# Kernel optimization log

Hardware: AMD Instinct MI355X
Metric: run time of the kernel (lower is better)

The kernel has to match this reference:

```python
import jax, jax.numpy as jnp
import numpy as np

N, D = 8192, 1024
TEMPERATURE = 0.1
EPS = 1e-8

def setup_inputs() -> dict:
    key = jax.random.key(0)
    k1, k2 = jax.random.split(key)
    emb = jax.random.normal(k1, (N, D), dtype=jnp.float32)
    # docstring: embeddings are normalized
    emb = emb / jnp.linalg.norm(emb, axis=1, keepdims=True)
    labels = jax.random.randint(k2, (N,), 0, 2, dtype=jnp.int32)
    return {"embeddings": emb, "labels": labels}

def reference(embeddings, labels):
    lab = labels.astype(embeddings.dtype)            # (N,)
    sim = jnp.matmul(embeddings, embeddings.T) / TEMPERATURE  # (N, N)
    exp_sim = jnp.exp(sim)                           # original uses raw exp (no max-subtract)
    diag = jnp.diagonal(exp_sim)                     # self-similarity exp(1/T)
    # all_sim excludes self; pos_sim = other reference rows (labels==1, j != i)
    all_sum = exp_sim.sum(axis=1) - diag             # (N,)
    pos_sum = exp_sim @ lab - diag * lab             # subtract self only when i is ref
    loss_per_row = -jnp.log(pos_sum / (all_sum + EPS))
    n_ref = lab.sum()
    loss = jnp.sum(jnp.where(lab > 0, loss_per_row, 0.0)) / jnp.maximum(n_ref, 1.0)
    # original returns 0.0 when fewer than 2 reference rows
    return jnp.where(n_ref < 2, jnp.array(0.0, embeddings.dtype), loss)
```

## Files before the change

kernel.cpp:

```cpp
#include <hip/hip_runtime.h>
#include <hip/hip_bf16.h>
#include <cstdint>
#include <cstddef>

#define NROWS 8192
#define DIM   1024
#define BM 128
#define BN 128
#define BK 64
#define INV_T 10.0f
#define EPS 1e-8f

typedef short  bf16x8  __attribute__((ext_vector_type(8)));
typedef float  floatx4 __attribute__((ext_vector_type(4)));

typedef __attribute__((address_space(1))) const void CGV;
typedef __attribute__((address_space(3))) void LV;

__device__ __forceinline__ void async_load16(const void* g, void* l) {
    __builtin_amdgcn_global_load_lds((CGV*)g, (LV*)l, 16, 0, 0);
}

__device__ __forceinline__ unsigned short f2bf_rne(float f) {
    union { float f; unsigned u; } c; c.f = f;
    unsigned u = c.u;
    unsigned r = (u + 0x7fffu + ((u >> 16) & 1u)) >> 16;
    return (unsigned short)r;
}

__global__ __launch_bounds__(256) void convert_kernel(
    const float* __restrict__ in, unsigned short* __restrict__ out)
{
    int i = (blockIdx.x * 256 + threadIdx.x) * 4;
    float4 v = *(const float4*)(in + i);
    ushort4 o;
    o.x = f2bf_rne(v.x);
    o.y = f2bf_rne(v.y);
    o.z = f2bf_rne(v.z);
    o.w = f2bf_rne(v.w);
    *(ushort4*)(out + i) = o;
}

__global__ __launch_bounds__(256, 4) void gemm_fused_kernel(
    const unsigned short* __restrict__ E,
    const int*            __restrict__ labels,
    float*                __restrict__ all_sum,
    float*                __restrict__ pos_sum)
{
    __shared__ __align__(16) unsigned short sA[BM * BK];
    __shared__ __align__(16) unsigned short sB[BN * BK];

    const int tid  = threadIdx.x;
    const int lane = tid & 63;
    const int w    = tid >> 6;
    const int wm   = w >> 1;
    const int wn   = w & 1;
    const int colw = lane & 15;
    const int quad = lane >> 4;

    const int t = blockIdx.x;
    int bi = (int)((sqrtf(8.0f * (float)t + 1.0f) - 1.0f) * 0.5f);
    while ((bi + 1) * (bi + 2) / 2 <= t) ++bi;
    while (bi * (bi + 1) / 2 > t) --bi;
    const int bj = t - bi * (bi + 1) / 2;

    const int rBase = bi * BM;
    const int cBase = bj * BN;
    const bool diag = (bi == bj);

    const int srow  = tid >> 3;
    const int scol  = (((tid & 7) ^ (srow & 7)) << 3);
    const int e0    = tid * 8;

    floatx4 acc[4][4];
    #pragma unroll
    for (int i = 0; i < 4; ++i)
        #pragma unroll
        for (int j = 0; j < 4; ++j)
            acc[i][j] = (floatx4)0.0f;

    const int swz   = colw & 7;
    const int aRow0 = (wm * 64 + colw) * BK;
    const int bRow0 = (wn * 64 + colw) * BK;

    const size_t gA0 = (size_t)(rBase + srow) * DIM + scol;
    const size_t gB0 = (size_t)(cBase + srow) * DIM + scol;
    const size_t rstep = (size_t)32 * DIM;

    for (int k0 = 0; k0 < DIM; k0 += BK) {
        __syncthreads();
        async_load16(E + gA0 + k0,             &sA[e0]);
        async_load16(E + gA0 + rstep + k0,     &sA[e0 + 2048]);
        async_load16(E + gA0 + 2 * rstep + k0, &sA[e0 + 4096]);
        async_load16(E + gA0 + 3 * rstep + k0, &sA[e0 + 6144]);
        async_load16(E + gB0 + k0,             &sB[e0]);
        async_load16(E + gB0 + rstep + k0,     &sB[e0 + 2048]);
        async_load16(E + gB0 + 2 * rstep + k0, &sB[e0 + 4096]);
        async_load16(E + gB0 + 3 * rstep + k0, &sB[e0 + 6144]);
        __syncthreads();

        #pragma unroll
        for (int h = 0; h < 2; ++h) {
            const int cOff = (((h << 2) | quad) ^ swz) << 3;
            bf16x8 aF[4], bF[4];
            #pragma unroll
            for (int mt = 0; mt < 4; ++mt)
                aF[mt] = *(const bf16x8*)&sA[aRow0 + mt * 16 * BK + cOff];
            #pragma unroll
            for (int nt = 0; nt < 4; ++nt)
                bF[nt] = *(const bf16x8*)&sB[bRow0 + nt * 16 * BK + cOff];

            #pragma unroll
            for (int mt = 0; mt < 4; ++mt)
                #pragma unroll
                for (int nt = 0; nt < 4; ++nt)
                    acc[mt][nt] = __builtin_amdgcn_mfma_f32_16x16x32_bf16(
                        aF[mt], bF[nt], acc[mt][nt], 0, 0, 0);
        }
    }

    float labc[4];
    int   gcol[4];
    #pragma unroll
    for (int nt = 0; nt < 4; ++nt) {
        gcol[nt] = cBase + wn * 64 + nt * 16 + colw;
        labc[nt] = (float)labels[gcol[nt]];
    }

    float colAll[4] = {0.f, 0.f, 0.f, 0.f};
    float colPos[4] = {0.f, 0.f, 0.f, 0.f};

    #pragma unroll
    for (int mt = 0; mt < 4; ++mt) {
        const int growBase = rBase + wm * 64 + mt * 16 + quad * 4;
        #pragma unroll
        for (int r = 0; r < 4; ++r) {
            const int grow = growBase + r;
            const float labr = (float)labels[grow];
            float sAll = 0.f, sPos = 0.f;
            #pragma unroll
            for (int nt = 0; nt < 4; ++nt) {
                float ev = __expf(acc[mt][nt][r] * INV_T);
                if (diag && grow == gcol[nt]) ev = 0.0f;
                sAll += ev;
                sPos += ev * labc[nt];
                colAll[nt] += ev;
                colPos[nt] += ev * labr;
            }
            #pragma unroll
            for (int off = 1; off < 16; off <<= 1) {
                sAll += __shfl_xor(sAll, off);
                sPos += __shfl_xor(sPos, off);
            }
            if (colw == 0) {
                atomicAdd(&all_sum[grow], sAll);
                atomicAdd(&pos_sum[grow], sPos);
            }
        }
    }

    if (!diag) {
        #pragma unroll
        for (int nt = 0; nt < 4; ++nt) {
            float a = colAll[nt], p = colPos[nt];
            a += __shfl_xor(a, 16);  p += __shfl_xor(p, 16);
            a += __shfl_xor(a, 32);  p += __shfl_xor(p, 32);
            if (quad == 0) {
                atomicAdd(&all_sum[gcol[nt]], a);
                atomicAdd(&pos_sum[gcol[nt]], p);
            }
        }
    }
}

__global__ __launch_bounds__(1024) void finalize_kernel(
    const float* __restrict__ all_sum,
    const float* __restrict__ pos_sum,
    const int*   __restrict__ labels,
    float*       __restrict__ out)
{
    __shared__ float sSum[1024];
    __shared__ float sCnt[1024];
    const int tid = threadIdx.x;
    float lsum = 0.f, lcnt = 0.f;
    for (int i = tid; i < NROWS; i += 1024) {
        if (labels[i] > 0) {
            float p = pos_sum[i];
            float a = all_sum[i] + EPS;
            lsum += -logf(p / a);
            lcnt += 1.0f;
        }
    }
    sSum[tid] = lsum;
    sCnt[tid] = lcnt;
    __syncthreads();
    for (int s = 512; s > 0; s >>= 1) {
        if (tid < s) { sSum[tid] += sSum[tid + s]; sCnt[tid] += sCnt[tid + s]; }
        __syncthreads();
    }
    if (tid == 0) {
        float n = sCnt[0];
        out[0] = (n < 2.0f) ? 0.0f : sSum[0] / fmaxf(n, 1.0f);
    }
}

extern "C" void kernel_launch(void* const* d_in, const int* in_sizes, int n_in,
                              void* d_out, int out_size, void* d_ws, size_t ws_size,
                              hipStream_t stream) {
    const float* emb    = (const float*)d_in[0];
    const int*   labels = (const int*)d_in[1];
    float*       out    = (float*)d_out;

    unsigned short* Ebf = (unsigned short*)d_ws;
    const size_t embBytes = (size_t)NROWS * DIM * sizeof(unsigned short);
    float* all_sum = (float*)((char*)d_ws + embBytes);
    float* pos_sum = all_sum + NROWS;

    hipMemsetAsync(all_sum, 0, 2 * NROWS * sizeof(float), stream);

    convert_kernel<<<(NROWS * DIM) / (4 * 256), 256, 0, stream>>>(emb, Ebf);

    const int nBlocksTri = (NROWS / BM) * (NROWS / BM + 1) / 2;
    gemm_fused_kernel<<<nBlocksTri, 256, 0, stream>>>(Ebf, labels, all_sum, pos_sum);

    finalize_kernel<<<1, 1024, 0, stream>>>(all_sum, pos_sum, labels, out);
}
```

Measured before the change: 217.5 us.

## Double-buffer LDS tiles with smaller K step and fold accumulator zeroing into convert

The GEMM main loop now keeps two LDS buffers with a K step of 32 instead of 64. It issues the async global-to-LDS loads for the next tile before computing on the current one, using one barrier per iteration instead of two, and the load/read swizzle is reworked to fit the narrower tile. The separate memset of the row-sum accumulators is removed; the convert kernel zeroes them instead, saving one stream operation. In exchange there are twice as many K iterations and barriers, and correctness depends on the barrier waiting for the outstanding async LDS loads.

Result: slower. 235.7 us (+8.4%).

```diff
diff --git a/kernel.cpp b/kernel.cpp
--- a/kernel.cpp
+++ b/kernel.cpp
@@ -7,7 +7,7 @@
 #define DIM   1024
 #define BM 128
 #define BN 128
-#define BK 64
+#define BK 32
 #define INV_T 10.0f
 #define EPS 1e-8f
 
@@ -29,7 +29,8 @@
 }
 
 __global__ __launch_bounds__(256) void convert_kernel(
-    const float* __restrict__ in, unsigned short* __restrict__ out)
+    const float* __restrict__ in, unsigned short* __restrict__ out,
+    float* __restrict__ accum )
 {
     int i = (blockIdx.x * 256 + threadIdx.x) * 4;
     float4 v = *(const float4*)(in + i);
@@ -39,6 +40,8 @@
     o.z = f2bf_rne(v.z);
     o.w = f2bf_rne(v.w);
     *(ushort4*)(out + i) = o;
+    if (blockIdx.x < (2 * NROWS) / 256)
+        accum[blockIdx.x * 256 + threadIdx.x] = 0.0f;
 }
 
 __global__ __launch_bounds__(256, 4) void gemm_fused_kernel(
@@ -47,8 +50,8 @@
     float*                __restrict__ all_sum,
     float*                __restrict__ pos_sum)
 {
-    __shared__ __align__(16) unsigned short sA[BM * BK];
-    __shared__ __align__(16) unsigned short sB[BN * BK];
+    __shared__ __align__(16) unsigned short sA[2][BM * BK];
+    __shared__ __align__(16) unsigned short sB[2][BN * BK];
 
     const int tid  = threadIdx.x;
     const int lane = tid & 63;
@@ -68,9 +71,9 @@
     const int cBase = bj * BN;
     const bool diag = (bi == bj);
 
-    const int srow  = tid >> 3;
-    const int scol  = (((tid & 7) ^ (srow & 7)) << 3);
-    const int e0    = tid * 8;
+    const int srow = tid >> 2;
+    const int scol = (((tid & 3) ^ ((tid >> 3) & 3)) << 3);
+    const int e0   = tid * 8;
 
     floatx4 acc[4][4];
     #pragma unroll
@@ -79,44 +82,46 @@
         for (int j = 0; j < 4; ++j)
             acc[i][j] = (floatx4)0.0f;
 
-    const int swz   = colw & 7;
+    const int swz   = (colw >> 1) & 3;
+    const int cOff  = ((quad ^ swz) << 3);
     const int aRow0 = (wm * 64 + colw) * BK;
     const int bRow0 = (wn * 64 + colw) * BK;
 
     const size_t gA0 = (size_t)(rBase + srow) * DIM + scol;
     const size_t gB0 = (size_t)(cBase + srow) * DIM + scol;
-    const size_t rstep = (size_t)32 * DIM;
-
-    for (int k0 = 0; k0 < DIM; k0 += BK) {
+    const size_t rstep = (size_t)64 * DIM;
+
+    async_load16(E + gA0,         &sA[0][e0]);
+    async_load16(E + gA0 + rstep, &sA[0][e0 + 2048]);
+    async_load16(E + gB0,         &sB[0][e0]);
+    async_load16(E + gB0 + rstep, &sB[0][e0 + 2048]);
+
+    #pragma unroll 2
+    for (int it = 0; it < DIM / BK; ++it) {
+        const int cur = it & 1;
         __syncthreads();
-        async_load16(E + gA0 + k0,             &sA[e0]);
-        async_load16(E + gA0 + rstep + k0,     &sA[e0 + 2048]);
-        async_load16(E + gA0 + 2 * rstep + k0, &sA[e0 + 4096]);
-        async_load16(E + gA0 + 3 * rstep + k0, &sA[e0 + 6144]);
-        async_load16(E + gB0 + k0,             &sB[e0]);
-        async_load16(E + gB0 + rstep + k0,     &sB[e0 + 2048]);
-        async_load16(E + gB0 + 2 * rstep + k0, &sB[e0 + 4096]);
-        async_load16(E + gB0 + 3 * rstep + k0, &sB[e0 + 6144]);
-        __syncthreads();
-
-        #pragma unroll
-        for (int h = 0; h < 2; ++h) {
-            const int cOff = (((h << 2) | quad) ^ swz) << 3;
-            bf16x8 aF[4], bF[4];
-            #pragma unroll
-            for (int mt = 0; mt < 4; ++mt)
-                aF[mt] = *(const bf16x8*)&sA[aRow0 + mt * 16 * BK + cOff];
+        if (it + 1 < DIM / BK) {
+            const size_t kOff = (size_t)(it + 1) * BK;
+            async_load16(E + gA0 + kOff,         &sA[1 - cur][e0]);
+            async_load16(E + gA0 + rstep + kOff, &sA[1 - cur][e0 + 2048]);
+            async_load16(E + gB0 + kOff,         &sB[1 - cur][e0]);
+            async_load16(E + gB0 + rstep + kOff, &sB[1 - cur][e0 + 2048]);
+        }
+
+        bf16x8 aF[4], bF[4];
+        #pragma unroll
+        for (int mt = 0; mt < 4; ++mt)
+            aF[mt] = *(const bf16x8*)&sA[cur][aRow0 + mt * 16 * BK + cOff];
+        #pragma unroll
+        for (int nt = 0; nt < 4; ++nt)
+            bF[nt] = *(const bf16x8*)&sB[cur][bRow0 + nt * 16 * BK + cOff];
+
+        #pragma unroll
+        for (int mt = 0; mt < 4; ++mt)
             #pragma unroll
             for (int nt = 0; nt < 4; ++nt)
-                bF[nt] = *(const bf16x8*)&sB[bRow0 + nt * 16 * BK + cOff];
-
-            #pragma unroll
-            for (int mt = 0; mt < 4; ++mt)
-                #pragma unroll
-                for (int nt = 0; nt < 4; ++nt)
-                    acc[mt][nt] = __builtin_amdgcn_mfma_f32_16x16x32_bf16(
-                        aF[mt], bF[nt], acc[mt][nt], 0, 0, 0);
-        }
+                acc[mt][nt] = __builtin_amdgcn_mfma_f32_16x16x32_bf16(
+                    aF[mt], bF[nt], acc[mt][nt], 0, 0, 0);
     }
 
     float labc[4];
@@ -216,9 +221,7 @@
     float* all_sum = (float*)((char*)d_ws + embBytes);
     float* pos_sum = all_sum + NROWS;
 
-    hipMemsetAsync(all_sum, 0, 2 * NROWS * sizeof(float), stream);
-
-    convert_kernel<<<(NROWS * DIM) / (4 * 256), 256, 0, stream>>>(emb, Ebf);
+    convert_kernel<<<(NROWS * DIM) / (4 * 256), 256, 0, stream>>>(emb, Ebf, all_sum);
 
     const int nBlocksTri = (NROWS / BM) * (NROWS / BM + 1) / 2;
     gemm_fused_kernel<<<nBlocksTri, 256, 0, stream>>>(Ebf, labels, all_sum, pos_sum);
```

## Register-prefetch GEMM tiles, fold memset into convert, prescale for exp2

Applied to the files above, without the earlier changes.

Replaces direct global-to-LDS async loads with register-staged prefetching of the next K tile while the current tile is computed, using explicit barriers. Folds the temperature scaling into a sqrt-prescale of the bf16 embeddings so the epilogue uses exp2 without a multiply. Zeroes the accumulators inside the convert kernel instead of a separate memset, and lowers occupancy hint to 3 waves per SIMD to afford extra registers. Prescaling before bf16 rounding slightly changes numerics, and register staging raises register pressure.

After: 213.9 us. No clear change (-1.6%).

```diff
diff --git a/kernel.cpp b/kernel.cpp
--- a/kernel.cpp
+++ b/kernel.cpp
@@ -8,18 +8,12 @@
 #define BM 128
 #define BN 128
 #define BK 64
-#define INV_T 10.0f
+#define NITER (DIM / BK)
 #define EPS 1e-8f
+#define PRESCALE 3.798283f
 
 typedef short  bf16x8  __attribute__((ext_vector_type(8)));
 typedef float  floatx4 __attribute__((ext_vector_type(4)));
-
-typedef __attribute__((address_space(1))) const void CGV;
-typedef __attribute__((address_space(3))) void LV;
-
-__device__ __forceinline__ void async_load16(const void* g, void* l) {
-    __builtin_amdgcn_global_load_lds((CGV*)g, (LV*)l, 16, 0, 0);
-}
 
 __device__ __forceinline__ unsigned short f2bf_rne(float f) {
     union { float f; unsigned u; } c; c.f = f;
@@ -29,19 +23,22 @@
 }
 
 __global__ __launch_bounds__(256) void convert_kernel(
-    const float* __restrict__ in, unsigned short* __restrict__ out)
+    const float* __restrict__ in, unsigned short* __restrict__ out,
+    float* __restrict__ accum )
 {
     int i = (blockIdx.x * 256 + threadIdx.x) * 4;
     float4 v = *(const float4*)(in + i);
     ushort4 o;
-    o.x = f2bf_rne(v.x);
-    o.y = f2bf_rne(v.y);
-    o.z = f2bf_rne(v.z);
-    o.w = f2bf_rne(v.w);
+    o.x = f2bf_rne(v.x * PRESCALE);
+    o.y = f2bf_rne(v.y * PRESCALE);
+    o.z = f2bf_rne(v.z * PRESCALE);
+    o.w = f2bf_rne(v.w * PRESCALE);
     *(ushort4*)(out + i) = o;
-}
-
-__global__ __launch_bounds__(256, 4) void gemm_fused_kernel(
+    if (blockIdx.x < (2 * NROWS) / 256)
+        accum[blockIdx.x * 256 + threadIdx.x] = 0.0f;
+}
+
+__global__ __launch_bounds__(256, 3) void gemm_fused_kernel(
     const unsigned short* __restrict__ E,
     const int*            __restrict__ labels,
     float*                __restrict__ all_sum,
@@ -68,9 +65,9 @@
     const int cBase = bj * BN;
     const bool diag = (bi == bj);
 
-    const int srow  = tid >> 3;
-    const int scol  = (((tid & 7) ^ (srow & 7)) << 3);
-    const int e0    = tid * 8;
+    const int srow = tid >> 3;
+    const int scol = (((tid & 7) ^ (srow & 7)) << 3);
+    const int e0   = tid * 8;
 
     floatx4 acc[4][4];
     #pragma unroll
@@ -87,17 +84,30 @@
     const size_t gB0 = (size_t)(cBase + srow) * DIM + scol;
     const size_t rstep = (size_t)32 * DIM;
 
-    for (int k0 = 0; k0 < DIM; k0 += BK) {
-        __syncthreads();
-        async_load16(E + gA0 + k0,             &sA[e0]);
-        async_load16(E + gA0 + rstep + k0,     &sA[e0 + 2048]);
-        async_load16(E + gA0 + 2 * rstep + k0, &sA[e0 + 4096]);
-        async_load16(E + gA0 + 3 * rstep + k0, &sA[e0 + 6144]);
-        async_load16(E + gB0 + k0,             &sB[e0]);
-        async_load16(E + gB0 + rstep + k0,     &sB[e0 + 2048]);
-        async_load16(E + gB0 + 2 * rstep + k0, &sB[e0 + 4096]);
-        async_load16(E + gB0 + 3 * rstep + k0, &sB[e0 + 6144]);
-        __syncthreads();
+    bf16x8 rA[4], rB[4];
+
+    #pragma unroll
+    for (int j = 0; j < 4; ++j) {
+        rA[j] = *(const bf16x8*)(E + gA0 + j * rstep);
+        rB[j] = *(const bf16x8*)(E + gB0 + j * rstep);
+    }
+
+    #pragma unroll
+    for (int it = 0; it < NITER; ++it) {
+        #pragma unroll
+        for (int j = 0; j < 4; ++j) {
+            *(bf16x8*)&sA[e0 + j * 2048] = rA[j];
+            *(bf16x8*)&sB[e0 + j * 2048] = rB[j];
+        }
+        if (it + 1 < NITER) {
+            const size_t kOff = (size_t)(it + 1) * BK;
+            #pragma unroll
+            for (int j = 0; j < 4; ++j) {
+                rA[j] = *(const bf16x8*)(E + gA0 + j * rstep + kOff);
+                rB[j] = *(const bf16x8*)(E + gB0 + j * rstep + kOff);
+            }
+        }
+        asm volatile("s_waitcnt lgkmcnt(0)\n\ts_barrier" ::: "memory");
 
         #pragma unroll
         for (int h = 0; h < 2; ++h) {
@@ -117,6 +127,8 @@
                     acc[mt][nt] = __builtin_amdgcn_mfma_f32_16x16x32_bf16(
                         aF[mt], bF[nt], acc[mt][nt], 0, 0, 0);
         }
+        if (it + 1 < NITER)
+            asm volatile("s_barrier" ::: "memory");
     }
 
     float labc[4];
@@ -140,7 +152,7 @@
             float sAll = 0.f, sPos = 0.f;
             #pragma unroll
             for (int nt = 0; nt < 4; ++nt) {
-                float ev = __expf(acc[mt][nt][r] * INV_T);
+                float ev = exp2f(acc[mt][nt][r]);
                 if (diag && grow == gcol[nt]) ev = 0.0f;
                 sAll += ev;
                 sPos += ev * labc[nt];
@@ -216,9 +228,7 @@
     float* all_sum = (float*)((char*)d_ws + embBytes);
     float* pos_sum = all_sum + NROWS;
 
-    hipMemsetAsync(all_sum, 0, 2 * NROWS * sizeof(float), stream);
-
-    convert_kernel<<<(NROWS * DIM) / (4 * 256), 256, 0, stream>>>(emb, Ebf);
+    convert_kernel<<<(NROWS * DIM) / (4 * 256), 256, 0, stream>>>(emb, Ebf, all_sum);
 
     const int nBlocksTri = (NROWS / BM) * (NROWS / BM + 1) / 2;
     gemm_fused_kernel<<<nBlocksTri, 256, 0, stream>>>(Ebf, labels, all_sum, pos_sum);
```
